# Optimization experiments

Measured on AMD Instinct MI355X. Metric: run time of the kernel, lower is better.

## Reference

```python
import jax, jax.numpy as jnp
import numpy as np

N_NODES = 50000
N_EDGES = 800000
N_REL = 4
D_IN = 128
D_OUT = 128


def setup_inputs() -> dict:
    key = jax.random.key(0)
    ks = jax.random.split(key, 7)
    X = jax.random.normal(ks[0], (N_NODES, D_IN), dtype=jnp.float32)
    rows = jax.random.randint(ks[1], (N_REL, N_EDGES), 0, N_NODES, dtype=jnp.int64)
    cols = jax.random.randint(ks[2], (N_REL, N_EDGES), 0, N_NODES, dtype=jnp.int64)
    vals = jax.random.uniform(ks[3], (N_REL, N_EDGES), dtype=jnp.float32)
    W_rel = jax.random.normal(ks[4], (N_REL, D_IN, D_OUT), dtype=jnp.float32) * (1.0 / np.sqrt(D_IN))
    W_self = jax.random.normal(ks[5], (D_IN, D_OUT), dtype=jnp.float32) * (1.0 / np.sqrt(D_IN))
    bias = jax.random.normal(ks[6], (D_OUT,), dtype=jnp.float32) * 0.01
    return {"X": X, "rows": rows, "cols": cols, "vals": vals,
            "W_rel": W_rel, "W_self": W_self, "bias": bias}


def reference(X, rows, cols, vals, W_rel, W_self, bias):
    """MedGCN multi-relation graph conv: out = X@W_self + sum_r norm(A_r)@X@W_r + b.

    Each A_r given as COO edge list (rows[r], cols[r], vals[r]); duplicate
    indices are summed (matching torch coalesce semantics).
    """
    n = X.shape[0]
    out = X @ W_self + bias
    for r in range(W_rel.shape[0]):
        i, j, v = rows[r], cols[r], vals[r]
        # D^{-1/2} A D^{-1/2}: deg[i] = sum_j A[i, j]
        deg = jax.ops.segment_sum(v, i, num_segments=n)
        inv_sqrt = jnp.clip(deg, 1e-12) ** -0.5
        v_norm = v * inv_sqrt[i] * inv_sqrt[j]
        # spmm: (A_norm @ X)[i] = sum over edges with row i of v_norm * X[j]
        AX = jax.ops.segment_sum(v_norm[:, None] * X[j], i, num_segments=n)
        out = out + AX @ W_rel[r]
    return out
```

## Files before the change

### kernel.cpp

```cpp
#include <hip/hip_runtime.h>
#include <hip/hip_bf16.h>

#define N_NODES 50000
#define N_EDGES 800000
#define N_REL   4
#define D       128
#define NE      (N_REL * N_EDGES)

#define S_SEG   64
#define SEG_E   (NE / S_SEG)
#define G_RANGES 8
#define RPG     (N_NODES / G_RANGES)

#define NCNT    (N_NODES * S_SEG)
#define SCAN_CHUNK 4096
#define NBLK ((NCNT + SCAN_CHUNK - 1) / SCAN_CHUNK)

#define OFF_BST   0
#define OFF_BSUM  12800000
#define OFF_BOFF  12803200
#define OFF_SORT  12806400
#define OFF_Y     38406400
#define OFF_RANK  89606400
#define OFF_INV2  96006400

typedef __attribute__((ext_vector_type(8))) short bf16x8;
typedef __attribute__((ext_vector_type(4))) float f32x4;

__device__ inline unsigned short f2bf(float f) {
    unsigned u = __float_as_uint(f);
    u += 0x7fffu + ((u >> 16) & 1u);
    return (unsigned short)(u >> 16);
}

__global__ __launch_bounds__(256) void k_prep_w(const float* __restrict__ Wself,
                                                const float* __restrict__ Wrel,
                                                unsigned short* __restrict__ Wt) {
    int id = blockIdx.x * 256 + threadIdx.x;
    int seg = id >> 14;
    int rem = id & 16383;
    int n = rem >> 7, k = rem & 127;
    float v = (seg == 0) ? Wself[k * 128 + n] : Wrel[(size_t)(seg - 1) * 16384 + k * 128 + n];
    Wt[id] = f2bf(v);
}

__global__ __launch_bounds__(256) void k_mm(const float* __restrict__ X,
                                            const unsigned short* __restrict__ Wt,
                                            const float* __restrict__ bias,
                                            float* __restrict__ out,
                                            unsigned short* __restrict__ Yb) {
    const int m0 = blockIdx.x * 64;
    const int tid = threadIdx.x;
    const int wave = tid >> 6, lane = tid & 63;
    const int wm = wave >> 1, wn = wave & 1;

    __shared__ unsigned short Xs[64][136];

#pragma unroll
    for (int l = 0; l < 8; l++) {
        int c = tid + l * 256;
        int row = c >> 5, c4 = c & 31;
        int gr = m0 + row;
        float4 v = make_float4(0.f, 0.f, 0.f, 0.f);
        if (gr < N_NODES) v = *(const float4*)(X + (size_t)gr * 128 + c4 * 4);
        ushort4 h;
        h.x = f2bf(v.x); h.y = f2bf(v.y); h.z = f2bf(v.z); h.w = f2bf(v.w);
        *(ushort4*)&Xs[row][c4 * 4] = h;
    }
    __syncthreads();

    const int lr = lane & 15;
    const int kb = (lane >> 4) * 8;
    const int lrow = (lane >> 4) * 4;
    const int lcol = lane & 15;
    const f32x4 zero = {0.f, 0.f, 0.f, 0.f};

    for (int seg = 0; seg < 5; seg++) {
        const unsigned short* Wseg = Wt + (size_t)seg * 16384;
        f32x4 acc[2][4];
#pragma unroll
        for (int i = 0; i < 2; i++)
#pragma unroll
            for (int j = 0; j < 4; j++) acc[i][j] = zero;

#pragma unroll
        for (int k0 = 0; k0 < 128; k0 += 32) {
            bf16x8 a[2], b[4];
#pragma unroll
            for (int i = 0; i < 2; i++)
                a[i] = *(const bf16x8*)&Xs[wm * 32 + i * 16 + lr][k0 + kb];
#pragma unroll
            for (int j = 0; j < 4; j++)
                b[j] = *(const bf16x8*)(Wseg + (size_t)(wn * 64 + j * 16 + lr) * 128 + k0 + kb);
#pragma unroll
            for (int i = 0; i < 2; i++)
#pragma unroll
                for (int j = 0; j < 4; j++)
                    acc[i][j] = __builtin_amdgcn_mfma_f32_16x16x32_bf16(a[i], b[j], acc[i][j], 0, 0, 0);
        }

        if (seg == 0) {
#pragma unroll
            for (int i = 0; i < 2; i++) {
#pragma unroll
                for (int j = 0; j < 4; j++) {
                    int gc = wn * 64 + j * 16 + lcol;
                    float bv = bias[gc];
#pragma unroll
                    for (int v = 0; v < 4; v++) {
                        int gr = m0 + wm * 32 + i * 16 + lrow + v;
                        if (gr < N_NODES)
                            out[(size_t)gr * 128 + gc] = acc[i][j][v] + bv;
                    }
                }
            }
        } else {
            unsigned short* Yseg = Yb + (size_t)(seg - 1) * N_NODES * 128;
#pragma unroll
            for (int i = 0; i < 2; i++) {
#pragma unroll
                for (int j = 0; j < 4; j++) {
                    int gc = wn * 64 + j * 16 + lcol;
#pragma unroll
                    for (int v = 0; v < 4; v++) {
                        int gr = m0 + wm * 32 + i * 16 + lrow + v;
                        if (gr < N_NODES)
                            Yseg[(size_t)gr * 128 + gc] = f2bf(acc[i][j][v]);
                    }
                }
            }
        }
    }
}

__global__ __launch_bounds__(256) void k_count(const int* __restrict__ rows,
                                               const float* __restrict__ vals,
                                               int* __restrict__ cntt,
                                               float* __restrict__ degt,
                                               unsigned short* __restrict__ rank) {
    __shared__ int lc[RPG];
    __shared__ float ld[RPG];
    const int seg = blockIdx.x >> 3;
    const int g = blockIdx.x & 7;
    const int rbase = g * RPG;
    for (int i = threadIdx.x; i < RPG; i += 256) { lc[i] = 0; ld[i] = 0.f; }
    __syncthreads();
    const int4* r4 = (const int4*)(rows + (size_t)seg * SEG_E);
    const float4* v4 = (const float4*)(vals + (size_t)seg * SEG_E);
    const int n4 = SEG_E / 4;
    for (int i = threadIdx.x; i < n4; i += 256) {
        int4 v = r4[i];
        float4 w = v4[i];
        int t = seg * SEG_E + i * 4;
        unsigned int l0 = (unsigned int)(v.x - rbase);
        unsigned int l1 = (unsigned int)(v.y - rbase);
        unsigned int l2 = (unsigned int)(v.z - rbase);
        unsigned int l3 = (unsigned int)(v.w - rbase);
        if (l0 < (unsigned int)RPG) { rank[t]     = (unsigned short)atomicAdd(&lc[l0], 1); atomicAdd(&ld[l0], w.x); }
        if (l1 < (unsigned int)RPG) { rank[t + 1] = (unsigned short)atomicAdd(&lc[l1], 1); atomicAdd(&ld[l1], w.y); }
        if (l2 < (unsigned int)RPG) { rank[t + 2] = (unsigned short)atomicAdd(&lc[l2], 1); atomicAdd(&ld[l2], w.z); }
        if (l3 < (unsigned int)RPG) { rank[t + 3] = (unsigned short)atomicAdd(&lc[l3], 1); atomicAdd(&ld[l3], w.w); }
    }
    __syncthreads();
    for (int i = threadIdx.x; i < RPG; i += 256) {
        cntt[(size_t)seg * N_NODES + rbase + i] = lc[i];
        degt[(size_t)seg * N_NODES + rbase + i] = ld[i];
    }
}

__global__ __launch_bounds__(256) void k_tr(const int* __restrict__ cntt,
                                            const float* __restrict__ degt,
                                            int* __restrict__ bst,
                                            float* __restrict__ inv2) {
    __shared__ int tile[64][65];
    __shared__ float dtile[64][65];
    const int r0 = blockIdx.x * 64;
    const int l = threadIdx.x & 63;
    const int q = threadIdx.x >> 6;
#pragma unroll
    for (int p = 0; p < 16; ++p) {
        int seg = q * 16 + p;
        int row = r0 + l;
        tile[seg][l] = (row < N_NODES) ? cntt[(size_t)seg * N_NODES + row] : 0;
        dtile[seg][l] = (row < N_NODES) ? degt[(size_t)seg * N_NODES + row] : 0.f;
    }
    __syncthreads();
#pragma unroll
    for (int p = 0; p < 16; ++p) {
        int rr = q * 16 + p;
        int row = r0 + rr;
        if (row < N_NODES) bst[(size_t)row * S_SEG + l] = tile[l][rr];
    }
    int rowl = threadIdx.x >> 2, rel = threadIdx.x & 3;
    int row = r0 + rowl;
    if (row < N_NODES) {
        float s = 0.f;
#pragma unroll
        for (int k = 0; k < 16; ++k) s += dtile[rel * 16 + k][rowl];
        inv2[(size_t)row * 4 + rel] = rsqrtf(fmaxf(s, 1e-12f));
    }
}

__global__ __launch_bounds__(256) void k_scanA(int* __restrict__ bst,
                                               int* __restrict__ bsum) {
    __shared__ int s[256];
    int t = threadIdx.x;
    int base = blockIdx.x * SCAN_CHUNK + t * 16;
    int4 v[4];
    int tsum = 0;
#pragma unroll
    for (int q = 0; q < 4; ++q) {
        int idx = base + q * 4;
        if (idx < NCNT) v[q] = *(const int4*)(bst + idx);
        else v[q] = make_int4(0, 0, 0, 0);
        tsum += v[q].x + v[q].y + v[q].z + v[q].w;
    }
    s[t] = tsum;
    __syncthreads();
    for (int off = 1; off < 256; off <<= 1) {
        int x = (t >= off) ? s[t - off] : 0;
        __syncthreads();
        s[t] += x;
        __syncthreads();
    }
    int run = s[t] - tsum;
#pragma unroll
    for (int q = 0; q < 4; ++q) {
        int idx = base + q * 4;
        if (idx < NCNT) {
            int4 o;
            o.x = run; run += v[q].x;
            o.y = run; run += v[q].y;
            o.z = run; run += v[q].z;
            o.w = run; run += v[q].w;
            *(int4*)(bst + idx) = o;
        }
    }
    if (t == 255) bsum[blockIdx.x] = s[255];
}

__global__ __launch_bounds__(256) void k_scanB(const int* __restrict__ bsum,
                                               int* __restrict__ boff) {
    __shared__ int s[256];
    int t = threadIdx.x;
    int b = t * 4;
    int v0 = (b     < NBLK) ? bsum[b]     : 0;
    int v1 = (b + 1 < NBLK) ? bsum[b + 1] : 0;
    int v2 = (b + 2 < NBLK) ? bsum[b + 2] : 0;
    int v3 = (b + 3 < NBLK) ? bsum[b + 3] : 0;
    int tsum = v0 + v1 + v2 + v3;
    s[t] = tsum;
    __syncthreads();
    for (int off = 1; off < 256; off <<= 1) {
        int x = (t >= off) ? s[t - off] : 0;
        __syncthreads();
        s[t] += x;
        __syncthreads();
    }
    int excl = s[t] - tsum;
    if (b     < NBLK) boff[b]     = excl;
    if (b + 1 < NBLK) boff[b + 1] = excl + v0;
    if (b + 2 < NBLK) boff[b + 2] = excl + v0 + v1;
    if (b + 3 < NBLK) boff[b + 3] = excl + v0 + v1 + v2;
}

__global__ __launch_bounds__(256) void k_scanC(int* __restrict__ bst,
                                               const int* __restrict__ boff) {
    int t = threadIdx.x;
    int base = blockIdx.x * SCAN_CHUNK + t * 16;
    int add = boff[blockIdx.x];
#pragma unroll
    for (int q = 0; q < 4; ++q) {
        int idx = base + q * 4;
        if (idx < NCNT) {
            int4 v = *(const int4*)(bst + idx);
            v.x += add; v.y += add; v.z += add; v.w += add;
            *(int4*)(bst + idx) = v;
        }
    }
}

__global__ __launch_bounds__(256) void k_fill(const int* __restrict__ rows,
                                              const int* __restrict__ cols,
                                              const float* __restrict__ vals,
                                              const int* __restrict__ bst,
                                              const unsigned short* __restrict__ rank,
                                              const float* __restrict__ inv2,
                                              unsigned int* __restrict__ erec) {
    int t = blockIdx.x * 256 + threadIdx.x;
    if (t >= NE) return;
    int seg = t / SEG_E;
    int r = seg >> 4;
    int row = rows[t], col = cols[t];
    float coef = vals[t] * inv2[(size_t)row * 4 + r] * inv2[(size_t)col * 4 + r];
    int pos = bst[(size_t)row * S_SEG + seg] + (int)rank[t];
    erec[pos] = ((unsigned int)f2bf(coef) << 16) | (unsigned int)col;
}

__global__ __launch_bounds__(256, 8) void k_gather(const int* __restrict__ bst,
                                                   const unsigned int* __restrict__ erec,
                                                   const unsigned int* __restrict__ Y2,
                                                   float* __restrict__ out) {
    const int wid = threadIdx.x >> 6;
    const int lane = threadIdx.x & 63;
    const int row = blockIdx.x * 4 + wid;
    if (row >= N_NODES) return;

    const int bend = (row + 1 < N_NODES) ? bst[(size_t)(row + 1) * S_SEG] : NE;

    float ax = 0.f, ay = 0.f;
#pragma unroll
    for (int rel = 0; rel < 4; ++rel) {
        const unsigned int* Yr = Y2 + (size_t)rel * N_NODES * 64;
        const int s = bst[(size_t)row * S_SEG + rel * 16];
        const int e = (rel < 3) ? bst[(size_t)row * S_SEG + rel * 16 + 16] : bend;
        for (int base = s; base < e; base += 64) {
            int rem = e - base;
            if (rem > 64) rem = 64;
            unsigned int recL = (lane < rem) ? erec[base + lane] : 0u;
            int c = 0;
            for (; c + 8 <= rem; c += 8) {
                unsigned int y[8];
                float cf[8];
#pragma unroll
                for (int j = 0; j < 8; ++j) {
                    unsigned int u = (unsigned int)__builtin_amdgcn_readlane((int)recL, c + j);
                    cf[j] = __uint_as_float(u & 0xffff0000u);
                    y[j] = Yr[(size_t)(u & 0xffffu) * 64 + lane];
                }
#pragma unroll
                for (int j = 0; j < 8; ++j) {
                    ax = fmaf(cf[j], __uint_as_float(y[j] << 16), ax);
                    ay = fmaf(cf[j], __uint_as_float(y[j] & 0xffff0000u), ay);
                }
            }
            for (; c < rem; ++c) {
                unsigned int u = (unsigned int)__builtin_amdgcn_readlane((int)recL, c);
                float cf = __uint_as_float(u & 0xffff0000u);
                unsigned int y = Yr[(size_t)(u & 0xffffu) * 64 + lane];
                ax = fmaf(cf, __uint_as_float(y << 16), ax);
                ay = fmaf(cf, __uint_as_float(y & 0xffff0000u), ay);
            }
        }
    }
    float2* op = (float2*)(out + (size_t)row * D) + lane;
    float2 o = *op;
    o.x += ax;
    o.y += ay;
    *op = o;
}

extern "C" void kernel_launch(void* const* d_in, const int* in_sizes, int n_in,
                              void* d_out, int out_size, void* d_ws, size_t ws_size,
                              hipStream_t stream) {
    const float* X     = (const float*)d_in[0];
    const int*   rows  = (const int*)d_in[1];
    const int*   cols  = (const int*)d_in[2];
    const float* vals  = (const float*)d_in[3];
    const float* Wrel  = (const float*)d_in[4];
    const float* Wself = (const float*)d_in[5];
    const float* bias  = (const float*)d_in[6];
    float* out = (float*)d_out;

    char* ws = (char*)d_ws;
    int*   bst  = (int*)(ws + OFF_BST);
    int*   bsum = (int*)(ws + OFF_BSUM);
    int*   boff = (int*)(ws + OFF_BOFF);
    unsigned short* Wt = (unsigned short*)(ws + OFF_SORT);
    int*   cntt = (int*)(ws + OFF_SORT);
    float* degt = (float*)(ws + OFF_SORT + 12800000);
    unsigned int* erec = (unsigned int*)(ws + OFF_SORT);
    unsigned short* Yb = (unsigned short*)(ws + OFF_Y);
    unsigned short* rank = (unsigned short*)(ws + OFF_RANK);
    float* inv2 = (float*)(ws + OFF_INV2);

    k_prep_w<<<320, 256, 0, stream>>>(Wself, Wrel, Wt);

    k_mm<<<(N_NODES + 63) / 64, 256, 0, stream>>>(X, Wt, bias, out, Yb);

    k_count<<<S_SEG * G_RANGES, 256, 0, stream>>>(rows, vals, cntt, degt, rank);
    k_tr<<<(N_NODES + 63) / 64, 256, 0, stream>>>(cntt, degt, bst, inv2);
    k_scanA<<<NBLK, 256, 0, stream>>>(bst, bsum);
    k_scanB<<<1, 256, 0, stream>>>(bsum, boff);
    k_scanC<<<NBLK, 256, 0, stream>>>(bst, boff);

    k_fill<<<(NE + 255) / 256, 256, 0, stream>>>(rows, cols, vals, bst, rank, inv2, erec);
    k_gather<<<(N_NODES + 3) / 4, 256, 0, stream>>>(bst, erec,
                                                    (const unsigned int*)Yb, out);
}
```

Measured before the change: 352.2 us.

## Compute degrees from sorted edges, transpose bucket offsets, enlarge GEMM tile

Degree accumulation moves out of the shared-memory atomic counting kernel into a pass over the CSR-sorted edge records, and a separate kernel then rewrites each edge's coefficient with the normalisation. A transposed copy of the bucket-start table lets the fill kernel read offsets in a segment-major, more coalesced layout. The dense GEMM tile grows from 64 to 128 rows per block. The trade is two extra kernels plus another read/write pass over the edge records. Degrees are now summed from bf16-rounded values, which changes the numerics slightly.

New measurement: 324.1 us. 8.0% less time.

```diff
diff --git a/kernel.cpp b/kernel.cpp
--- a/kernel.cpp
+++ b/kernel.cpp
@@ -20,6 +20,7 @@
 #define OFF_BSUM  12800000
 #define OFF_BOFF  12803200
 #define OFF_SORT  12806400
+#define OFF_BSTT  (12806400 + 12800000)
 #define OFF_Y     38406400
 #define OFF_RANK  89606400
 #define OFF_INV2  96006400
@@ -49,15 +50,15 @@
                                             const float* __restrict__ bias,
                                             float* __restrict__ out,
                                             unsigned short* __restrict__ Yb) {
-    const int m0 = blockIdx.x * 64;
+    const int m0 = blockIdx.x * 128;
     const int tid = threadIdx.x;
     const int wave = tid >> 6, lane = tid & 63;
     const int wm = wave >> 1, wn = wave & 1;
 
-    __shared__ unsigned short Xs[64][136];
-
-#pragma unroll
-    for (int l = 0; l < 8; l++) {
+    __shared__ unsigned short Xs[128][136];
+
+#pragma unroll
+    for (int l = 0; l < 16; l++) {
         int c = tid + l * 256;
         int row = c >> 5, c4 = c & 31;
         int gr = m0 + row;
@@ -77,23 +78,23 @@
 
     for (int seg = 0; seg < 5; seg++) {
         const unsigned short* Wseg = Wt + (size_t)seg * 16384;
-        f32x4 acc[2][4];
-#pragma unroll
-        for (int i = 0; i < 2; i++)
+        f32x4 acc[4][4];
+#pragma unroll
+        for (int i = 0; i < 4; i++)
 #pragma unroll
             for (int j = 0; j < 4; j++) acc[i][j] = zero;
 
 #pragma unroll
         for (int k0 = 0; k0 < 128; k0 += 32) {
-            bf16x8 a[2], b[4];
-#pragma unroll
-            for (int i = 0; i < 2; i++)
-                a[i] = *(const bf16x8*)&Xs[wm * 32 + i * 16 + lr][k0 + kb];
+            bf16x8 a[4], b[4];
+#pragma unroll
+            for (int i = 0; i < 4; i++)
+                a[i] = *(const bf16x8*)&Xs[wm * 64 + i * 16 + lr][k0 + kb];
 #pragma unroll
             for (int j = 0; j < 4; j++)
                 b[j] = *(const bf16x8*)(Wseg + (size_t)(wn * 64 + j * 16 + lr) * 128 + k0 + kb);
 #pragma unroll
-            for (int i = 0; i < 2; i++)
+            for (int i = 0; i < 4; i++)
 #pragma unroll
                 for (int j = 0; j < 4; j++)
                     acc[i][j] = __builtin_amdgcn_mfma_f32_16x16x32_bf16(a[i], b[j], acc[i][j], 0, 0, 0);
@@ -101,14 +102,14 @@
 
         if (seg == 0) {
 #pragma unroll
-            for (int i = 0; i < 2; i++) {
+            for (int i = 0; i < 4; i++) {
 #pragma unroll
                 for (int j = 0; j < 4; j++) {
                     int gc = wn * 64 + j * 16 + lcol;
                     float bv = bias[gc];
 #pragma unroll
                     for (int v = 0; v < 4; v++) {
-                        int gr = m0 + wm * 32 + i * 16 + lrow + v;
+                        int gr = m0 + wm * 64 + i * 16 + lrow + v;
                         if (gr < N_NODES)
                             out[(size_t)gr * 128 + gc] = acc[i][j][v] + bv;
                     }
@@ -117,13 +118,13 @@
         } else {
             unsigned short* Yseg = Yb + (size_t)(seg - 1) * N_NODES * 128;
 #pragma unroll
-            for (int i = 0; i < 2; i++) {
+            for (int i = 0; i < 4; i++) {
 #pragma unroll
                 for (int j = 0; j < 4; j++) {
                     int gc = wn * 64 + j * 16 + lcol;
 #pragma unroll
                     for (int v = 0; v < 4; v++) {
-                        int gr = m0 + wm * 32 + i * 16 + lrow + v;
+                        int gr = m0 + wm * 64 + i * 16 + lrow + v;
                         if (gr < N_NODES)
                             Yseg[(size_t)gr * 128 + gc] = f2bf(acc[i][j][v]);
                     }
@@ -134,46 +135,36 @@
 }
 
 __global__ __launch_bounds__(256) void k_count(const int* __restrict__ rows,
-                                               const float* __restrict__ vals,
                                                int* __restrict__ cntt,
-                                               float* __restrict__ degt,
                                                unsigned short* __restrict__ rank) {
     __shared__ int lc[RPG];
-    __shared__ float ld[RPG];
     const int seg = blockIdx.x >> 3;
     const int g = blockIdx.x & 7;
     const int rbase = g * RPG;
-    for (int i = threadIdx.x; i < RPG; i += 256) { lc[i] = 0; ld[i] = 0.f; }
+    for (int i = threadIdx.x; i < RPG; i += 256) lc[i] = 0;
     __syncthreads();
     const int4* r4 = (const int4*)(rows + (size_t)seg * SEG_E);
-    const float4* v4 = (const float4*)(vals + (size_t)seg * SEG_E);
     const int n4 = SEG_E / 4;
     for (int i = threadIdx.x; i < n4; i += 256) {
         int4 v = r4[i];
-        float4 w = v4[i];
         int t = seg * SEG_E + i * 4;
         unsigned int l0 = (unsigned int)(v.x - rbase);
         unsigned int l1 = (unsigned int)(v.y - rbase);
         unsigned int l2 = (unsigned int)(v.z - rbase);
         unsigned int l3 = (unsigned int)(v.w - rbase);
-        if (l0 < (unsigned int)RPG) { rank[t]     = (unsigned short)atomicAdd(&lc[l0], 1); atomicAdd(&ld[l0], w.x); }
-        if (l1 < (unsigned int)RPG) { rank[t + 1] = (unsigned short)atomicAdd(&lc[l1], 1); atomicAdd(&ld[l1], w.y); }
-        if (l2 < (unsigned int)RPG) { rank[t + 2] = (unsigned short)atomicAdd(&lc[l2], 1); atomicAdd(&ld[l2], w.z); }
-        if (l3 < (unsigned int)RPG) { rank[t + 3] = (unsigned short)atomicAdd(&lc[l3], 1); atomicAdd(&ld[l3], w.w); }
-    }
-    __syncthreads();
-    for (int i = threadIdx.x; i < RPG; i += 256) {
+        if (l0 < (unsigned int)RPG) rank[t]     = (unsigned short)atomicAdd(&lc[l0], 1);
+        if (l1 < (unsigned int)RPG) rank[t + 1] = (unsigned short)atomicAdd(&lc[l1], 1);
+        if (l2 < (unsigned int)RPG) rank[t + 2] = (unsigned short)atomicAdd(&lc[l2], 1);
+        if (l3 < (unsigned int)RPG) rank[t + 3] = (unsigned short)atomicAdd(&lc[l3], 1);
+    }
+    __syncthreads();
+    for (int i = threadIdx.x; i < RPG; i += 256)
         cntt[(size_t)seg * N_NODES + rbase + i] = lc[i];
-        degt[(size_t)seg * N_NODES + rbase + i] = ld[i];
-    }
 }
 
 __global__ __launch_bounds__(256) void k_tr(const int* __restrict__ cntt,
-                                            const float* __restrict__ degt,
-                                            int* __restrict__ bst,
-                                            float* __restrict__ inv2) {
+                                            int* __restrict__ bst) {
     __shared__ int tile[64][65];
-    __shared__ float dtile[64][65];
     const int r0 = blockIdx.x * 64;
     const int l = threadIdx.x & 63;
     const int q = threadIdx.x >> 6;
@@ -182,7 +173,6 @@
         int seg = q * 16 + p;
         int row = r0 + l;
         tile[seg][l] = (row < N_NODES) ? cntt[(size_t)seg * N_NODES + row] : 0;
-        dtile[seg][l] = (row < N_NODES) ? degt[(size_t)seg * N_NODES + row] : 0.f;
     }
     __syncthreads();
 #pragma unroll
@@ -190,14 +180,6 @@
         int rr = q * 16 + p;
         int row = r0 + rr;
         if (row < N_NODES) bst[(size_t)row * S_SEG + l] = tile[l][rr];
-    }
-    int rowl = threadIdx.x >> 2, rel = threadIdx.x & 3;
-    int row = r0 + rowl;
-    if (row < N_NODES) {
-        float s = 0.f;
-#pragma unroll
-        for (int k = 0; k < 16; ++k) s += dtile[rel * 16 + k][rowl];
-        inv2[(size_t)row * 4 + rel] = rsqrtf(fmaxf(s, 1e-12f));
     }
 }
 
@@ -280,21 +262,76 @@
     }
 }
 
+__global__ __launch_bounds__(256) void k_tr2(const int* __restrict__ bst,
+                                             int* __restrict__ bstt) {
+    __shared__ int tile[64][65];
+    const int r0 = blockIdx.x * 64;
+    const int l = threadIdx.x & 63;
+    const int q = threadIdx.x >> 6;
+#pragma unroll
+    for (int p = 0; p < 16; ++p) {
+        int rr = q * 16 + p;
+        int row = r0 + rr;
+        tile[rr][l] = (row < N_NODES) ? bst[(size_t)row * S_SEG + l] : 0;
+    }
+    __syncthreads();
+#pragma unroll
+    for (int p = 0; p < 16; ++p) {
+        int seg = q * 16 + p;
+        int row = r0 + l;
+        if (row < N_NODES) bstt[(size_t)seg * N_NODES + row] = tile[l][seg];
+    }
+}
+
 __global__ __launch_bounds__(256) void k_fill(const int* __restrict__ rows,
                                               const int* __restrict__ cols,
                                               const float* __restrict__ vals,
-                                              const int* __restrict__ bst,
+                                              const int* __restrict__ bstt,
                                               const unsigned short* __restrict__ rank,
-                                              const float* __restrict__ inv2,
                                               unsigned int* __restrict__ erec) {
     int t = blockIdx.x * 256 + threadIdx.x;
     if (t >= NE) return;
     int seg = t / SEG_E;
-    int r = seg >> 4;
     int row = rows[t], col = cols[t];
-    float coef = vals[t] * inv2[(size_t)row * 4 + r] * inv2[(size_t)col * 4 + r];
-    int pos = bst[(size_t)row * S_SEG + seg] + (int)rank[t];
-    erec[pos] = ((unsigned int)f2bf(coef) << 16) | (unsigned int)col;
+    int pos = bstt[(size_t)seg * N_NODES + row] + (int)rank[t];
+    erec[pos] = ((unsigned int)f2bf(vals[t]) << 16) | (unsigned int)col;
+}
+
+__global__ __launch_bounds__(256) void k_degc(const int* __restrict__ bst,
+                                              const unsigned int* __restrict__ erec,
+                                              float* __restrict__ inv2) {
+    int t = blockIdx.x * 256 + threadIdx.x;
+    if (t >= N_NODES * 4) return;
+    int row = t >> 2, rel = t & 3;
+    int s = bst[(size_t)row * S_SEG + rel * 16];
+    int e = (rel < 3) ? bst[(size_t)row * S_SEG + rel * 16 + 16]
+                      : ((row + 1 < N_NODES) ? bst[(size_t)(row + 1) * S_SEG] : NE);
+    float acc = 0.f;
+    for (int i = s; i < e; ++i) acc += __uint_as_float(erec[i] & 0xffff0000u);
+    inv2[t] = rsqrtf(fmaxf(acc, 1e-12f));
+}
+
+__global__ __launch_bounds__(256) void k_coef(const int* __restrict__ bst,
+                                              const float* __restrict__ inv2,
+                                              unsigned int* __restrict__ erec) {
+    const int wid = threadIdx.x >> 6;
+    const int lane = threadIdx.x & 63;
+    const int row = blockIdx.x * 4 + wid;
+    if (row >= N_NODES) return;
+    const int bend = (row + 1 < N_NODES) ? bst[(size_t)(row + 1) * S_SEG] : NE;
+#pragma unroll
+    for (int rel = 0; rel < 4; ++rel) {
+        const float si = inv2[(size_t)row * 4 + rel];
+        const int s = bst[(size_t)row * S_SEG + rel * 16];
+        const int e = (rel < 3) ? bst[(size_t)row * S_SEG + rel * 16 + 16] : bend;
+        for (int i = s + lane; i < e; i += 64) {
+            unsigned int u = erec[i];
+            unsigned int col = u & 0xffffu;
+            float val = __uint_as_float(u & 0xffff0000u);
+            float coef = val * si * inv2[(size_t)col * 4 + rel];
+            erec[i] = ((unsigned int)f2bf(coef) << 16) | col;
+        }
+    }
 }
 
 __global__ __launch_bounds__(256, 8) void k_gather(const int* __restrict__ bst,
@@ -368,23 +405,26 @@
     int*   boff = (int*)(ws + OFF_BOFF);
     unsigned short* Wt = (unsigned short*)(ws + OFF_SORT);
     int*   cntt = (int*)(ws + OFF_SORT);
-    float* degt = (float*)(ws + OFF_SORT + 12800000);
     unsigned int* erec = (unsigned int*)(ws + OFF_SORT);
+    int*   bstt = (int*)(ws + OFF_BSTT);
     unsigned short* Yb = (unsigned short*)(ws + OFF_Y);
     unsigned short* rank = (unsigned short*)(ws + OFF_RANK);
     float* inv2 = (float*)(ws + OFF_INV2);
 
     k_prep_w<<<320, 256, 0, stream>>>(Wself, Wrel, Wt);
 
-    k_mm<<<(N_NODES + 63) / 64, 256, 0, stream>>>(X, Wt, bias, out, Yb);
-
-    k_count<<<S_SEG * G_RANGES, 256, 0, stream>>>(rows, vals, cntt, degt, rank);
-    k_tr<<<(N_NODES + 63) / 64, 256, 0, stream>>>(cntt, degt, bst, inv2);
+    k_mm<<<(N_NODES + 127) / 128, 256, 0, stream>>>(X, Wt, bias, out, Yb);
+
+    k_count<<<S_SEG * G_RANGES, 256, 0, stream>>>(rows, cntt, rank);
+    k_tr<<<(N_NODES + 63) / 64, 256, 0, stream>>>(cntt, bst);
     k_scanA<<<NBLK, 256, 0, stream>>>(bst, bsum);
     k_scanB<<<1, 256, 0, stream>>>(bsum, boff);
     k_scanC<<<NBLK, 256, 0, stream>>>(bst, boff);
-
-    k_fill<<<(NE + 255) / 256, 256, 0, stream>>>(rows, cols, vals, bst, rank, inv2, erec);
+    k_tr2<<<(N_NODES + 63) / 64, 256, 0, stream>>>(bst, bstt);
+
+    k_fill<<<(NE + 255) / 256, 256, 0, stream>>>(rows, cols, vals, bstt, rank, erec);
+    k_degc<<<(N_NODES * 4 + 255) / 256, 256, 0, stream>>>(bst, erec, inv2);
+    k_coef<<<(N_NODES + 3) / 4, 256, 0, stream>>>(bst, inv2, erec);
     k_gather<<<(N_NODES + 3) / 4, 256, 0, stream>>>(bst, erec,
                                                     (const unsigned int*)Yb, out);
 }
```
